# Performance work log

Hardware: AMD Instinct MI355X
Metric: run time of the kernel (lower is better)

## Reference

```python
import jax, jax.numpy as jnp
import numpy as np

B, S, D = 1, 2048, 1024
H, KD = 16, 64          # heads, key_dim = hidden/heads
VD, HS = 2048, 128      # v_dim = 2*hidden (double_v_dim), head_size = v_dim/heads
EPS = 1e-5


def rotate_every_two(x):
    x1 = x[..., ::2]
    x2 = x[..., 1::2]
    return jnp.stack((-x2, x1), axis=-1).reshape(x.shape)


def setup_inputs() -> dict:
    key = jax.random.key(0)
    ks = jax.random.split(key, 8)
    x = jax.random.normal(ks[0], (B, S, D), jnp.float32)
    # rotary-style sin/cos, shape [S, KD]
    pos = jnp.arange(S, dtype=jnp.float32)
    inv_freq = 1.0 / (10000.0 ** (jnp.arange(0, KD, 2, dtype=jnp.float32) / KD))
    ang = jnp.repeat(pos[:, None] * inv_freq[None, :], 2, axis=-1)  # [S, KD]
    sin, cos = jnp.sin(ang), jnp.cos(ang)
    # RetNet per-head decay mask, shape [H, S, S]
    gammas = 1.0 - 2.0 ** (-5.0 - jnp.arange(H, dtype=jnp.float32))
    n = jnp.arange(S, dtype=jnp.float32)
    diff = n[:, None] - n[None, :]                    # [S, S]
    mask = jnp.where(diff >= 0, gammas[:, None, None] ** diff[None, :, :], 0.0)
    mask = mask / jnp.sqrt(jnp.sum(mask, axis=-1, keepdims=True))
    # projection weights stored [in, out] (equivalent to torch Linear W^T)
    gain = 2.0 ** (-2.5)
    Wq = gain * jax.random.normal(ks[1], (D, D), jnp.float32) * (2.0 / (D + D)) ** 0.5
    Wk = gain * jax.random.normal(ks[2], (D, D), jnp.float32) * (2.0 / (D + D)) ** 0.5
    Wv = gain * jax.random.normal(ks[3], (D, VD), jnp.float32) * (2.0 / (D + VD)) ** 0.5
    Wg = gain * jax.random.normal(ks[4], (D, VD), jnp.float32) * (2.0 / (D + VD)) ** 0.5
    Wo = jax.random.normal(ks[5], (VD, D), jnp.float32) * (2.0 / (VD + D)) ** 0.5
    gn_w = jnp.ones((VD,), jnp.float32)
    gn_b = jnp.zeros((VD,), jnp.float32)
    return {"x": x, "sin": sin, "cos": cos, "mask": mask,
            "Wq": Wq, "Wk": Wk, "Wv": Wv, "Wg": Wg, "Wo": Wo,
            "gn_w": gn_w, "gn_b": gn_b}


def reference(x, sin, cos, mask, Wq, Wk, Wv, Wg, Wo, gn_w, gn_b):
    scaling = KD ** (-0.5)
    q = (x @ Wq).reshape(B, S, H, KD).transpose(0, 2, 1, 3)            # [B,H,S,KD]
    k = ((x @ Wk) * scaling).reshape(B, S, H, KD).transpose(0, 2, 1, 3)
    v = x @ Wv                                                          # [B,S,VD]
    g = x @ Wg
    qr = q * cos + rotate_every_two(q) * sin                            # theta_shift
    kr = k * cos + rotate_every_two(k) * sin
    vr = v.reshape(B, S, H, HS).transpose(0, 2, 1, 3)                   # [B,H,S,HS]
    qk = jnp.einsum('bhsd,bhtd->bhst', qr, kr) * mask                  # [B,H,S,S]
    den = jnp.clip(jnp.abs(jax.lax.stop_gradient(qk).sum(-1, keepdims=True)), 1.0, None)
    o = jnp.einsum('bhst,bhtv->bhsv', qk / den, vr)                    # [B,H,S,HS]
    o = o.transpose(0, 2, 1, 3).reshape(S, H * HS)                      # bsz==1 reshape
    # GroupNorm(H groups over VD channels), rows are the batch dim
    og = o.reshape(S, H, HS)
    mu = og.mean(-1, keepdims=True)
    var = og.var(-1, keepdims=True)
    og = (og - mu) * jax.lax.rsqrt(var + EPS)
    o = (og * gn_w.reshape(H, HS) + gn_b.reshape(H, HS)).reshape(B, S, VD)
    out = (g * jax.nn.sigmoid(g)) * o                                   # swish gate
    return out @ Wo                                                     # [B,S,D]
```

## Files before the change

kernel.cpp:

```cpp
#include <hip/hip_runtime.h>
#include <cstdint>
#include <cstddef>

typedef unsigned short u16;
typedef u16   u16x8 __attribute__((ext_vector_type(8)));
typedef u16   u16x4 __attribute__((ext_vector_type(4)));
typedef u16   u16x2 __attribute__((ext_vector_type(2)));
typedef float f32x4 __attribute__((ext_vector_type(4)));

#define S_LEN 2048

static __device__ __forceinline__ u16 f2bf(float f){
  union { float f; unsigned u; } v; v.f = f;
  unsigned r = (v.u + 0x7FFFu + ((v.u >> 16) & 1u)) >> 16;
  return (u16)r;
}
static __device__ __forceinline__ float bf2f(u16 u){
  union { unsigned u; float f; } v; v.u = ((unsigned)u) << 16; return v.f;
}

static __device__ __forceinline__ void mfma16(f32x4& c, u16x8 a, u16x8 b){
  asm("s_nop 1\n\tv_mfma_f32_16x16x32_bf16 %0, %1, %2, %0"
      : "+v"(c) : "v"(a), "v"(b));
}

#if defined(__has_builtin)
#  if __has_builtin(__builtin_amdgcn_global_load_lds)
#    define USE_GLDS 1
#  endif
#endif

static __device__ __forceinline__ void stage16(const u16* g, u16* l){
#ifdef USE_GLDS
  __builtin_amdgcn_global_load_lds((const __attribute__((address_space(1))) void*)g,
                                   (__attribute__((address_space(3))) void*)l,
                                   16, 0, 0);
#else
  *(u16x8*)l = *(const u16x8*)g;
#endif
}

__global__ __launch_bounds__(256) void prep_all(
    const float* __restrict__ x, u16* __restrict__ xb,
    const float* __restrict__ Wq, const float* __restrict__ Wk,
    const float* __restrict__ Wv, const float* __restrict__ Wg,
    const float* __restrict__ Wo, u16* __restrict__ WT, u16* __restrict__ WoT){
  __shared__ float tile[32][33];
  int bid = blockIdx.x;
  if (bid >= 8192){
    int i = ((bid - 8192) * 256 + threadIdx.x) * 4;
    float4 v = *(const float4*)(x + i);
    u16x4 o; o[0] = f2bf(v.x); o[1] = f2bf(v.y); o[2] = f2bf(v.z); o[3] = f2bf(v.w);
    *(u16x4*)(xb + i) = o;
    return;
  }
  const float* W; u16* dst; int K, N, lb, lgx; float scale = 1.0f;
  if (bid < 1024)      { W=Wq; dst=WT;                        K=1024; N=1024; lb=bid;        lgx=5; }
  else if (bid < 2048) { W=Wk; dst=WT + (size_t)1024 * 1024;  K=1024; N=1024; lb=bid - 1024; lgx=5; scale=0.125f; }
  else if (bid < 4096) { W=Wv; dst=WT + (size_t)2048 * 1024;  K=1024; N=2048; lb=bid - 2048; lgx=6; }
  else if (bid < 6144) { W=Wg; dst=WT + (size_t)4096 * 1024;  K=1024; N=2048; lb=bid - 4096; lgx=6; }
  else                 { W=Wo; dst=WoT;                       K=2048; N=1024; lb=bid - 6144; lgx=5; }
  int n0 = (lb & ((1 << lgx) - 1)) * 32;
  int k0 = (lb >> lgx) * 32;
  int tx = threadIdx.x & 31, ty = threadIdx.x >> 5;
  #pragma unroll
  for (int i = 0; i < 32; i += 8)
    tile[ty + i][tx] = W[(size_t)(k0 + ty + i) * N + n0 + tx];
  __syncthreads();
  #pragma unroll
  for (int i = 0; i < 32; i += 8)
    dst[(size_t)(n0 + ty + i) * K + k0 + tx] = f2bf(scale * tile[tx][ty + i]);
}

template<int MODE, int BN>
__global__ __launch_bounds__(256) void gemm2(
    const u16* __restrict__ A, const u16* __restrict__ BT, int K,
    float* __restrict__ outF,
    u16* __restrict__ oq, u16* __restrict__ ok,
    u16* __restrict__ ovT, u16* __restrict__ og,
    const float* __restrict__ sinb, const float* __restrict__ cosb)
{
  constexpr int NI = BN / 32;
  constexpr int LB_LOADS = BN * 8 / 256;
  constexpr int TL = 4 + LB_LOADS;
  constexpr int LBOFF = 128 * 64;

  __shared__ u16 sh[2][128 * 64 + BN * 64];

  const int t = threadIdx.x;
  const int lane = t & 63, w = t >> 6;
  const int r = lane & 15, g4 = lane >> 4;
  const int bm = blockIdx.y * 128, bn = blockIdx.x * BN;
  const int wm = (w & 1) * 64, wn = (w >> 1) * (BN / 2);

  f32x4 acc[4][NI] = {};

  auto STAGE = [&](int buf, int kb){
    #pragma unroll
    for (int p = 0; p < 4; ++p){
      int ci = p * 256 + t;
      int row = ci >> 3, ch = ci & 7;
      stage16(A + (size_t)(bm + row) * K + kb + ((ch ^ (row & 7)) * 8),
              &sh[buf][ci * 8]);
    }
    #pragma unroll
    for (int p = 0; p < LB_LOADS; ++p){
      int ci = p * 256 + t;
      int row = ci >> 3, ch = ci & 7;
      stage16(BT + (size_t)(bn + row) * K + kb + ((ch ^ (row & 7)) * 8),
              &sh[buf][LBOFF + ci * 8]);
    }
  };

  STAGE(0, 0);
  int cur = 0;
  for (int kb = 0; kb < K; kb += 64){
    if (kb + 64 < K){
      STAGE(cur ^ 1, kb + 64);
      if constexpr (TL == 8) asm volatile("s_waitcnt vmcnt(8)" ::: "memory");
      else                   asm volatile("s_waitcnt vmcnt(6)" ::: "memory");
    } else {
      asm volatile("s_waitcnt vmcnt(0)" ::: "memory");
    }
    __builtin_amdgcn_s_barrier();

    #pragma unroll
    for (int j = 0; j < 2; ++j){
      u16x8 af[4], bfr[NI];
      #pragma unroll
      for (int i = 0; i < 4; ++i){
        int row = wm + 16 * i + r;
        af[i] = *(const u16x8*)&sh[cur][row * 64 + (((j * 4 + g4) ^ (row & 7)) * 8)];
      }
      #pragma unroll
      for (int i = 0; i < NI; ++i){
        int row = wn + 16 * i + r;
        bfr[i] = *(const u16x8*)&sh[cur][LBOFF + row * 64 + (((j * 4 + g4) ^ (row & 7)) * 8)];
      }
      #pragma unroll
      for (int mi = 0; mi < 4; ++mi)
        #pragma unroll
        for (int ni = 0; ni < NI; ++ni)
          mfma16(acc[mi][ni], af[mi], bfr[ni]);
    }
    asm volatile("s_waitcnt lgkmcnt(0)" ::: "memory");
    __builtin_amdgcn_s_barrier();
    cur ^= 1;
  }

  if constexpr (MODE == 2){
    #pragma unroll
    for (int mi = 0; mi < 4; ++mi)
      #pragma unroll
      for (int ni = 0; ni < NI; ++ni)
        #pragma unroll
        for (int rr = 0; rr < 4; ++rr){
          int row = bm + wm + 16 * mi + 4 * g4 + rr;
          int col = bn + wn + 16 * ni + r;
          outF[(size_t)row * 1024 + col] = acc[mi][ni][rr];
        }
  } else {
    u16* L = &sh[0][0];
    if (bn < 2048){
      constexpr int STR = 136;
      #pragma unroll
      for (int mi = 0; mi < 4; ++mi)
        #pragma unroll
        for (int ni = 0; ni < NI; ++ni){
          int nl = wn + 16 * ni + r;
          int n  = bn + nl;
          int kd = n & 63;
          #pragma unroll
          for (int rr = 0; rr < 4; ++rr){
            int sl = wm + 16 * mi + 4 * g4 + rr;
            int srow = bm + sl;
            float v = acc[mi][ni][rr];
            float pv = __shfl_xor(v, 1);
            float cs = cosb[srow * 64 + kd];
            float sn = sinb[srow * 64 + kd];
            float o = v * cs + ((n & 1) ? pv : -pv) * sn;
            L[sl * STR + nl] = f2bf(o);
          }
        }
      asm volatile("s_waitcnt lgkmcnt(0)" ::: "memory");
      __builtin_amdgcn_s_barrier();
      #pragma unroll
      for (int it = 0; it < 8; ++it){
        int id = it * 256 + t;
        int sl = id >> 4, c = id & 15, hb = c >> 3, kc = c & 7;
        u16x8 val = *(const u16x8*)&L[sl * STR + hb * 64 + kc * 8];
        int n0 = bn + hb * 64;
        u16* dst = (n0 < 1024)
          ? (oq + ((size_t)(n0 >> 6)          * S_LEN + bm + sl) * 64 + kc * 8)
          : (ok + ((size_t)((n0 - 1024) >> 6) * S_LEN + bm + sl) * 64 + kc * 8);
        *(u16x8*)dst = val;
      }
    } else if (bn < 4096){
      constexpr int STR = 137;
      #pragma unroll
      for (int mi = 0; mi < 4; ++mi)
        #pragma unroll
        for (int ni = 0; ni < NI; ++ni){
          int nl = wn + 16 * ni + r;
          #pragma unroll
          for (int rr = 0; rr < 4; ++rr){
            int sl = wm + 16 * mi + 4 * g4 + rr;
            L[sl * STR + nl] = f2bf(acc[mi][ni][rr]);
          }
        }
      asm volatile("s_waitcnt lgkmcnt(0)" ::: "memory");
      __builtin_amdgcn_s_barrier();
      #pragma unroll
      for (int it = 0; it < 8; ++it){
        int id = it * 256 + t;
        int nl = id >> 4, sc = id & 15;
        u16x8 pk;
        #pragma unroll
        for (int j = 0; j < 8; ++j)
          pk[j] = L[(sc * 8 + j) * STR + nl];
        *(u16x8*)&ovT[(size_t)(bn - 2048 + nl) * S_LEN + bm + sc * 8] = pk;
      }
    } else {
      constexpr int STR = 136;
      #pragma unroll
      for (int mi = 0; mi < 4; ++mi)
        #pragma unroll
        for (int ni = 0; ni < NI; ++ni){
          int nl = wn + 16 * ni + r;
          #pragma unroll
          for (int rr = 0; rr < 4; ++rr){
            int sl = wm + 16 * mi + 4 * g4 + rr;
            L[sl * STR + nl] = f2bf(acc[mi][ni][rr]);
          }
        }
      asm volatile("s_waitcnt lgkmcnt(0)" ::: "memory");
      __builtin_amdgcn_s_barrier();
      #pragma unroll
      for (int it = 0; it < 8; ++it){
        int id = it * 256 + t;
        int sl = id >> 4, c = id & 15;
        u16x8 val = *(const u16x8*)&L[sl * STR + c * 8];
        *(u16x8*)&og[(size_t)(bm + sl) * 2048 + (bn - 4096) + c * 8] = val;
      }
    }
  }
}

__global__ __launch_bounds__(256) void retention_gn(const u16* __restrict__ qrb,
                                                    const u16* __restrict__ krb,
                                                    const u16* __restrict__ vTb,
                                                    const u16* __restrict__ gbuf,
                                                    const float* __restrict__ gnw,
                                                    const float* __restrict__ gnb,
                                                    u16* __restrict__ gated){
  __shared__ u16 kt[2][64 * 64];
  __shared__ u16 vt[2][128 * 64];
  __shared__ u16 pb[4][16 * 88];

  const int idx = blockIdx.x;
  const int h  = idx & 15;
  const int sb = (idx < 256) ? (31 - (idx >> 4)) : ((idx >> 4) - 16);
  const int s0 = sb * 64;
  const int t  = threadIdx.x;
  const int w  = t >> 6, lane = t & 63;
  const int r  = lane & 15, g4 = lane >> 4;
  const int s0w = s0 + 16 * w;

  const float om   = exp2f(-5.0f - (float)h);
  const float lg   = logf(1.0f - om);
  const float l2g  = lg * 1.44269504088896f;
  const float dmax = 30.0f / (-l2g);

  int t0 = 0;
  {
    float tf = (float)(s0 - 63) - dmax;
    if (tf > 0.0f) t0 = ((int)tf) & ~63;
  }

  const u16* qrow = qrb + ((size_t)h * S_LEN + (s0w + r)) * 64 + 8 * g4;
  u16x8 qf0 = *(const u16x8*)(qrow);
  u16x8 qf1 = *(const u16x8*)(qrow + 32);

  float invn[4];
  #pragma unroll
  for (int rr = 0; rr < 4; ++rr){
    int s = s0w + 4 * g4 + rr;
    invn[rr] = rsqrtf(-expm1f((float)(s + 1) * lg) / om);
  }
  float bsub[4];
  {
    float e_r  = exp2f(-(float)r * l2g);
    float e16  = exp2f(-16.0f * l2g);
    bsub[0] = e_r; bsub[1] = bsub[0] * e16; bsub[2] = bsub[1] * e16; bsub[3] = bsub[2] * e16;
  }

  f32x4 oacc[8] = {};
  float rs[4] = {0.f, 0.f, 0.f, 0.f};

  auto STAGE = [&](int buf, int tb){
    #pragma unroll
    for (int p = 0; p < 2; ++p){
      int ci = p * 256 + t;
      int row = ci >> 3, ch = ci & 7;
      const u16* src = krb + ((size_t)h * S_LEN + tb + row) * 64 + ((ch ^ (row & 7)) * 8);
      stage16(src, &kt[buf][ci * 8]);
    }
    #pragma unroll
    for (int p = 0; p < 4; ++p){
      int ci = p * 256 + t;
      int row = ci >> 3, ch = ci & 7;
      const u16* src = vTb + ((size_t)(h * 128 + row)) * S_LEN + tb + ((ch ^ (row & 7)) * 8);
      stage16(src, &vt[buf][ci * 8]);
    }
  };

  STAGE(0, t0);
  int cur = 0;
  for (int tb = t0; tb <= s0; tb += 64){
    const bool last = (tb + 64 > s0);
    if (!last){
      STAGE(cur ^ 1, tb + 64);
      asm volatile("s_waitcnt vmcnt(6)" ::: "memory");
    } else {
      asm volatile("s_waitcnt vmcnt(0)" ::: "memory");
    }
    __builtin_amdgcn_s_barrier();

    if (tb <= s0w + 15 && (float)(s0w - tb - 63) <= dmax){
      f32x4 p[4] = {};
      #pragma unroll
      for (int sub = 0; sub < 4; ++sub){
        int row = 16 * sub + r;
        u16x8 kf0 = *(const u16x8*)&kt[cur][row * 64 + ((g4       ^ (row & 7)) * 8)];
        u16x8 kf1 = *(const u16x8*)&kt[cur][row * 64 + (((4 + g4) ^ (row & 7)) * 8)];
        mfma16(p[sub], qf0, kf0);
        mfma16(p[sub], qf1, kf1);
      }
      asm volatile("s_nop 7\n\ts_nop 7"
                   : "+v"(p[0]), "+v"(p[1]), "+v"(p[2]), "+v"(p[3]));
      float arr[4];
      #pragma unroll
      for (int rr = 0; rr < 4; ++rr)
        arr[rr] = exp2f((float)(s0w + 4 * g4 + rr - tb) * l2g) * invn[rr];
      #pragma unroll
      for (int sub = 0; sub < 4; ++sub){
        int tt = tb + 16 * sub + r;
        #pragma unroll
        for (int rr = 0; rr < 4; ++rr){
          int srow = s0w + 4 * g4 + rr;
          float dec = (srow >= tt) ? arr[rr] * bsub[sub] : 0.0f;
          float val = p[sub][rr] * dec;
          rs[rr] += val;
          pb[w][(4 * g4 + rr) * 88 + 16 * sub + r] = f2bf(val);
        }
      }
      asm volatile("s_waitcnt lgkmcnt(0)" ::: "memory");
      __builtin_amdgcn_sched_barrier(0);
      u16x8 pf0 = *(const u16x8*)&pb[w][r * 88 + 8 * g4];
      u16x8 pf1 = *(const u16x8*)&pb[w][r * 88 + 32 + 8 * g4];
      #pragma unroll
      for (int cs = 0; cs < 8; ++cs){
        int row = 16 * cs + r;
        u16x8 vf0 = *(const u16x8*)&vt[cur][row * 64 + ((g4       ^ (row & 7)) * 8)];
        u16x8 vf1 = *(const u16x8*)&vt[cur][row * 64 + (((4 + g4) ^ (row & 7)) * 8)];
        mfma16(oacc[cs], pf0, vf0);
        mfma16(oacc[cs], pf1, vf1);
      }
    }
    asm volatile("s_waitcnt lgkmcnt(0)" ::: "memory");
    __builtin_amdgcn_s_barrier();
    cur ^= 1;
  }

  #pragma unroll
  for (int rr = 0; rr < 4; ++rr){
    float v = rs[rr];
    v += __shfl_xor(v, 1); v += __shfl_xor(v, 2);
    v += __shfl_xor(v, 4); v += __shfl_xor(v, 8);
    float den = fabsf(v); if (den < 1.0f) den = 1.0f;
    rs[rr] = 1.0f / den;
  }

  float gw[8], gbv[8];
  #pragma unroll
  for (int cs = 0; cs < 8; ++cs){
    int gc = h * 128 + 16 * cs + r;
    gw[cs]  = gnw[gc];
    gbv[cs] = gnb[gc];
  }
  #pragma unroll
  for (int rr = 0; rr < 4; ++rr){
    int s = s0w + 4 * g4 + rr;
    float vv[8], m = 0.0f;
    #pragma unroll
    for (int cs = 0; cs < 8; ++cs){ vv[cs] = oacc[cs][rr] * rs[rr]; m += vv[cs]; }
    m += __shfl_xor(m, 1); m += __shfl_xor(m, 2);
    m += __shfl_xor(m, 4); m += __shfl_xor(m, 8);
    float mu = m * (1.0f / 128.0f);
    float sq = 0.0f;
    #pragma unroll
    for (int cs = 0; cs < 8; ++cs){ float d = vv[cs] - mu; sq += d * d; }
    sq += __shfl_xor(sq, 1); sq += __shfl_xor(sq, 2);
    sq += __shfl_xor(sq, 4); sq += __shfl_xor(sq, 8);
    float rstd = rsqrtf(sq * (1.0f / 128.0f) + 1e-5f);
    #pragma unroll
    for (int cs = 0; cs < 8; ++cs){
      int gc = h * 128 + 16 * cs + r;
      float nv = (vv[cs] - mu) * rstd * gw[cs] + gbv[cs];
      float gv = bf2f(gbuf[(size_t)s * 2048 + gc]);
      float res = gv / (1.0f + __expf(-gv)) * nv;
      gated[(size_t)s * 2048 + gc] = f2bf(res);
    }
  }
}

extern "C" void kernel_launch(void* const* d_in, const int* in_sizes, int n_in,
                              void* d_out, int out_size, void* d_ws, size_t ws_size,
                              hipStream_t stream)
{
  (void)in_sizes; (void)n_in; (void)out_size; (void)ws_size;
  const float* x    = (const float*)d_in[0];
  const float* sinb = (const float*)d_in[1];
  const float* cosb = (const float*)d_in[2];
  const float* Wq   = (const float*)d_in[4];
  const float* Wk   = (const float*)d_in[5];
  const float* Wv   = (const float*)d_in[6];
  const float* Wg   = (const float*)d_in[7];
  const float* Wo   = (const float*)d_in[8];
  const float* gnw  = (const float*)d_in[9];
  const float* gnb  = (const float*)d_in[10];
  float* out = (float*)d_out;

  char* ws = (char*)d_ws;
  u16*   xb    = (u16*)  (ws + 0);
  u16*   WT    = (u16*)  (ws + ((size_t)4  << 20));
  u16*   gated = (u16*)  (ws + 0);
  u16*   WoT   = (u16*)  (ws + ((size_t)16 << 20));
  u16*   qrb   = (u16*)  (ws + ((size_t)20 << 20));
  u16*   krb   = (u16*)  (ws + ((size_t)24 << 20));
  u16*   vTb   = (u16*)  (ws + ((size_t)28 << 20));
  u16*   gbuf  = (u16*)  (ws + ((size_t)36 << 20));

  prep_all<<<dim3(10240), dim3(256), 0, stream>>>(x, xb, Wq, Wk, Wv, Wg, Wo, WT, WoT);

  gemm2<0, 128><<<dim3(48, 16), dim3(256), 0, stream>>>(xb, WT, 1024,
      nullptr, qrb, krb, vTb, gbuf, sinb, cosb);

  retention_gn<<<dim3(512), dim3(256), 0, stream>>>(qrb, krb, vTb, gbuf, gnw, gnb, gated);

  gemm2<2, 64><<<dim3(16, 16), dim3(256), 0, stream>>>(gated, WoT, 2048,
      out, nullptr, nullptr, nullptr, nullptr, nullptr, nullptr);
}
```

Before: 121.3 us.

## Use two waves per retention block, each handling 32 query rows

The retention kernel now runs 128 threads (two waves) per block instead of four, with each wave processing two 16-row query subtiles. Each K and V fragment read from LDS therefore feeds twice as many MFMAs, which cuts LDS traffic per unit of compute. In exchange, each thread issues more staging loads (the vmcnt wait is adjusted to match), register pressure rises from the doubled accumulators, and there are fewer waves available to hide latency.

```diff
diff --git a/kernel.cpp b/kernel.cpp
--- a/kernel.cpp
+++ b/kernel.cpp
@@ -246,7 +246,7 @@
   }
 }
 
-__global__ __launch_bounds__(256) void retention_gn(const u16* __restrict__ qrb,
+__global__ __launch_bounds__(128) void retention_gn(const u16* __restrict__ qrb,
                                                     const u16* __restrict__ krb,
                                                     const u16* __restrict__ vTb,
                                                     const u16* __restrict__ gbuf,
@@ -255,7 +255,7 @@
                                                     u16* __restrict__ gated){
   __shared__ u16 kt[2][64 * 64];
   __shared__ u16 vt[2][128 * 64];
-  __shared__ u16 pb[4][16 * 88];
+  __shared__ u16 pb[2][2][16 * 88];
 
   const int idx = blockIdx.x;
   const int h  = idx & 15;
@@ -264,7 +264,7 @@
   const int t  = threadIdx.x;
   const int w  = t >> 6, lane = t & 63;
   const int r  = lane & 15, g4 = lane >> 4;
-  const int s0w = s0 + 16 * w;
+  const int s0w = s0 + 32 * w;
 
   const float om   = exp2f(-5.0f - (float)h);
   const float lg   = logf(1.0f - om);
@@ -277,16 +277,22 @@
     if (tf > 0.0f) t0 = ((int)tf) & ~63;
   }
 
-  const u16* qrow = qrb + ((size_t)h * S_LEN + (s0w + r)) * 64 + 8 * g4;
-  u16x8 qf0 = *(const u16x8*)(qrow);
-  u16x8 qf1 = *(const u16x8*)(qrow + 32);
-
-  float invn[4];
-  #pragma unroll
-  for (int rr = 0; rr < 4; ++rr){
-    int s = s0w + 4 * g4 + rr;
-    invn[rr] = rsqrtf(-expm1f((float)(s + 1) * lg) / om);
-  }
+  u16x8 qf[2][2];
+  #pragma unroll
+  for (int st = 0; st < 2; ++st){
+    const u16* qrow = qrb + ((size_t)h * S_LEN + (s0w + 16 * st + r)) * 64 + 8 * g4;
+    qf[st][0] = *(const u16x8*)(qrow);
+    qf[st][1] = *(const u16x8*)(qrow + 32);
+  }
+
+  float invn[2][4];
+  #pragma unroll
+  for (int st = 0; st < 2; ++st)
+    #pragma unroll
+    for (int rr = 0; rr < 4; ++rr){
+      int s = s0w + 16 * st + 4 * g4 + rr;
+      invn[st][rr] = rsqrtf(-expm1f((float)(s + 1) * lg) / om);
+    }
   float bsub[4];
   {
     float e_r  = exp2f(-(float)r * l2g);
@@ -294,20 +300,20 @@
     bsub[0] = e_r; bsub[1] = bsub[0] * e16; bsub[2] = bsub[1] * e16; bsub[3] = bsub[2] * e16;
   }
 
-  f32x4 oacc[8] = {};
-  float rs[4] = {0.f, 0.f, 0.f, 0.f};
+  f32x4 oacc[2][8] = {};
+  float rs[2][4] = {};
 
   auto STAGE = [&](int buf, int tb){
     #pragma unroll
-    for (int p = 0; p < 2; ++p){
-      int ci = p * 256 + t;
+    for (int p = 0; p < 4; ++p){
+      int ci = p * 128 + t;
       int row = ci >> 3, ch = ci & 7;
       const u16* src = krb + ((size_t)h * S_LEN + tb + row) * 64 + ((ch ^ (row & 7)) * 8);
       stage16(src, &kt[buf][ci * 8]);
     }
     #pragma unroll
-    for (int p = 0; p < 4; ++p){
-      int ci = p * 256 + t;
+    for (int p = 0; p < 8; ++p){
+      int ci = p * 128 + t;
       int row = ci >> 3, ch = ci & 7;
       const u16* src = vTb + ((size_t)(h * 128 + row)) * S_LEN + tb + ((ch ^ (row & 7)) * 8);
       stage16(src, &vt[buf][ci * 8]);
@@ -320,51 +326,64 @@
     const bool last = (tb + 64 > s0);
     if (!last){
       STAGE(cur ^ 1, tb + 64);
-      asm volatile("s_waitcnt vmcnt(6)" ::: "memory");
+      asm volatile("s_waitcnt vmcnt(12)" ::: "memory");
     } else {
       asm volatile("s_waitcnt vmcnt(0)" ::: "memory");
     }
     __builtin_amdgcn_s_barrier();
 
-    if (tb <= s0w + 15 && (float)(s0w - tb - 63) <= dmax){
-      f32x4 p[4] = {};
+    if (tb <= s0w + 31 && (float)(s0w - tb - 63) <= dmax){
+      f32x4 p[2][4] = {};
       #pragma unroll
       for (int sub = 0; sub < 4; ++sub){
         int row = 16 * sub + r;
         u16x8 kf0 = *(const u16x8*)&kt[cur][row * 64 + ((g4       ^ (row & 7)) * 8)];
         u16x8 kf1 = *(const u16x8*)&kt[cur][row * 64 + (((4 + g4) ^ (row & 7)) * 8)];
-        mfma16(p[sub], qf0, kf0);
-        mfma16(p[sub], qf1, kf1);
+        mfma16(p[0][sub], qf[0][0], kf0);
+        mfma16(p[0][sub], qf[0][1], kf1);
+        mfma16(p[1][sub], qf[1][0], kf0);
+        mfma16(p[1][sub], qf[1][1], kf1);
       }
       asm volatile("s_nop 7\n\ts_nop 7"
-                   : "+v"(p[0]), "+v"(p[1]), "+v"(p[2]), "+v"(p[3]));
-      float arr[4];
-      #pragma unroll
-      for (int rr = 0; rr < 4; ++rr)
-        arr[rr] = exp2f((float)(s0w + 4 * g4 + rr - tb) * l2g) * invn[rr];
-      #pragma unroll
-      for (int sub = 0; sub < 4; ++sub){
-        int tt = tb + 16 * sub + r;
-        #pragma unroll
-        for (int rr = 0; rr < 4; ++rr){
-          int srow = s0w + 4 * g4 + rr;
-          float dec = (srow >= tt) ? arr[rr] * bsub[sub] : 0.0f;
-          float val = p[sub][rr] * dec;
-          rs[rr] += val;
-          pb[w][(4 * g4 + rr) * 88 + 16 * sub + r] = f2bf(val);
+                   : "+v"(p[0][0]), "+v"(p[0][1]), "+v"(p[0][2]), "+v"(p[0][3]),
+                     "+v"(p[1][0]), "+v"(p[1][1]), "+v"(p[1][2]), "+v"(p[1][3]));
+      float arr[2][4];
+      #pragma unroll
+      for (int st = 0; st < 2; ++st)
+        #pragma unroll
+        for (int rr = 0; rr < 4; ++rr)
+          arr[st][rr] = exp2f((float)(s0w + 16 * st + 4 * g4 + rr - tb) * l2g) * invn[st][rr];
+      #pragma unroll
+      for (int st = 0; st < 2; ++st)
+        #pragma unroll
+        for (int sub = 0; sub < 4; ++sub){
+          int tt = tb + 16 * sub + r;
+          #pragma unroll
+          for (int rr = 0; rr < 4; ++rr){
+            int srow = s0w + 16 * st + 4 * g4 + rr;
+            float dec = (srow >= tt) ? arr[st][rr] * bsub[sub] : 0.0f;
+            float val = p[st][sub][rr] * dec;
+            rs[st][rr] += val;
+            pb[w][st][(4 * g4 + rr) * 88 + 16 * sub + r] = f2bf(val);
+          }
         }
-      }
       asm volatile("s_waitcnt lgkmcnt(0)" ::: "memory");
       __builtin_amdgcn_sched_barrier(0);
-      u16x8 pf0 = *(const u16x8*)&pb[w][r * 88 + 8 * g4];
-      u16x8 pf1 = *(const u16x8*)&pb[w][r * 88 + 32 + 8 * g4];
+      u16x8 pf[2][2];
+      #pragma unroll
+      for (int st = 0; st < 2; ++st){
+        pf[st][0] = *(const u16x8*)&pb[w][st][r * 88 + 8 * g4];
+        pf[st][1] = *(const u16x8*)&pb[w][st][r * 88 + 32 + 8 * g4];
+      }
       #pragma unroll
       for (int cs = 0; cs < 8; ++cs){
         int row = 16 * cs + r;
         u16x8 vf0 = *(const u16x8*)&vt[cur][row * 64 + ((g4       ^ (row & 7)) * 8)];
         u16x8 vf1 = *(const u16x8*)&vt[cur][row * 64 + (((4 + g4) ^ (row & 7)) * 8)];
-        mfma16(oacc[cs], pf0, vf0);
-        mfma16(oacc[cs], pf1, vf1);
+        mfma16(oacc[0][cs], pf[0][0], vf0);
+        mfma16(oacc[0][cs], pf[0][1], vf1);
+        mfma16(oacc[1][cs], pf[1][0], vf0);
+        mfma16(oacc[1][cs], pf[1][1], vf1);
       }
     }
     asm volatile("s_waitcnt lgkmcnt(0)" ::: "memory");
@@ -373,13 +392,15 @@
   }
 
   #pragma unroll
-  for (int rr = 0; rr < 4; ++rr){
-    float v = rs[rr];
-    v += __shfl_xor(v, 1); v += __shfl_xor(v, 2);
-    v += __shfl_xor(v, 4); v += __shfl_xor(v, 8);
-    float den = fabsf(v); if (den < 1.0f) den = 1.0f;
-    rs[rr] = 1.0f / den;
-  }
+  for (int st = 0; st < 2; ++st)
+    #pragma unroll
+    for (int rr = 0; rr < 4; ++rr){
+      float v = rs[st][rr];
+      v += __shfl_xor(v, 1); v += __shfl_xor(v, 2);
+      v += __shfl_xor(v, 4); v += __shfl_xor(v, 8);
+      float den = fabsf(v); if (den < 1.0f) den = 1.0f;
+      rs[st][rr] = 1.0f / den;
+    }
 
   float gw[8], gbv[8];
   #pragma unroll
@@ -389,29 +410,31 @@
     gbv[cs] = gnb[gc];
   }
   #pragma unroll
-  for (int rr = 0; rr < 4; ++rr){
-    int s = s0w + 4 * g4 + rr;
-    float vv[8], m = 0.0f;
-    #pragma unroll
-    for (int cs = 0; cs < 8; ++cs){ vv[cs] = oacc[cs][rr] * rs[rr]; m += vv[cs]; }
-    m += __shfl_xor(m, 1); m += __shfl_xor(m, 2);
-    m += __shfl_xor(m, 4); m += __shfl_xor(m, 8);
-    float mu = m * (1.0f / 128.0f);
-    float sq = 0.0f;
-    #pragma unroll
-    for (int cs = 0; cs < 8; ++cs){ float d = vv[cs] - mu; sq += d * d; }
-    sq += __shfl_xor(sq, 1); sq += __shfl_xor(sq, 2);
-    sq += __shfl_xor(sq, 4); sq += __shfl_xor(sq, 8);
-    float rstd = rsqrtf(sq * (1.0f / 128.0f) + 1e-5f);
-    #pragma unroll
-    for (int cs = 0; cs < 8; ++cs){
-      int gc = h * 128 + 16 * cs + r;
-      float nv = (vv[cs] - mu) * rstd * gw[cs] + gbv[cs];
-      float gv = bf2f(gbuf[(size_t)s * 2048 + gc]);
-      float res = gv / (1.0f + __expf(-gv)) * nv;
-      gated[(size_t)s * 2048 + gc] = f2bf(res);
-    }
-  }
+  for (int st = 0; st < 2; ++st)
+    #pragma unroll
+    for (int rr = 0; rr < 4; ++rr){
+      int s = s0w + 16 * st + 4 * g4 + rr;
+      float vv[8], m = 0.0f;
+      #pragma unroll
+      for (int cs = 0; cs < 8; ++cs){ vv[cs] = oacc[st][cs][rr] * rs[st][rr]; m += vv[cs]; }
+      m += __shfl_xor(m, 1); m += __shfl_xor(m, 2);
+      m += __shfl_xor(m, 4); m += __shfl_xor(m, 8);
+      float mu = m * (1.0f / 128.0f);
+      float sq = 0.0f;
+      #pragma unroll
+      for (int cs = 0; cs < 8; ++cs){ float d = vv[cs] - mu; sq += d * d; }
+      sq += __shfl_xor(sq, 1); sq += __shfl_xor(sq, 2);
+      sq += __shfl_xor(sq, 4); sq += __shfl_xor(sq, 8);
+      float rstd = rsqrtf(sq * (1.0f / 128.0f) + 1e-5f);
+      #pragma unroll
+      for (int cs = 0; cs < 8; ++cs){
+        int gc = h * 128 + 16 * cs + r;
+        float nv = (vv[cs] - mu) * rstd * gw[cs] + gbv[cs];
+        float gv = bf2f(gbuf[(size_t)s * 2048 + gc]);
+        float res = gv / (1.0f + __expf(-gv)) * nv;
+        gated[(size_t)s * 2048 + gc] = f2bf(res);
+      }
+    }
 }
 
 extern "C" void kernel_launch(void* const* d_in, const int* in_sizes, int n_in,
@@ -446,7 +469,7 @@
   gemm2<0, 128><<<dim3(48, 16), dim3(256), 0, stream>>>(xb, WT, 1024,
       nullptr, qrb, krb, vTb, gbuf, sinb, cosb);
 
-  retention_gn<<<dim3(512), dim3(256), 0, stream>>>(qrb, krb, vTb, gbuf, gnw, gnb, gated);
+  retention_gn<<<dim3(512), dim3(128), 0, stream>>>(qrb, krb, vTb, gbuf, gnw, gnb, gated);
 
   gemm2<2, 64><<<dim3(16, 16), dim3(256), 0, stream>>>(gated, WoT, 2048,
       out, nullptr, nullptr, nullptr, nullptr, nullptr, nullptr);
```

Measured after the change: 140.7 us. +16.0%, slower.
